# Kernel tuning notes

Measured on AMD Instinct MI355X. Metric: run time of the kernel, lower is better.

Reference implementation:

```python
import jax, jax.numpy as jnp
import numpy as np

OVERALL_W = (0.4, 0.4, 0.1, 0.1)


def nn_distance(pc1, pc2):
    # pc1: (B,N,3), pc2: (B,M,3) -> squared NN distance each way.
    # ||a-b||^2 = ||a||^2 + ||b||^2 - 2 a.b ; compute via batched GEMM.
    n1 = jnp.sum(pc1 * pc1, axis=-1)  # (B,N)
    n2 = jnp.sum(pc2 * pc2, axis=-1)  # (B,M)
    cross = jnp.einsum('bnd,bmd->bnm', pc1, pc2)  # (B,N,M)
    d = n1[:, :, None] + n2[:, None, :] - 2.0 * cross  # (B,N,M)
    dist1 = jnp.min(d, axis=2)  # (B,N)
    dist2 = jnp.min(d, axis=1)  # (B,M)
    return dist1, dist2


def setup_inputs() -> dict:
    key = jax.random.key(0)
    ks = jax.random.split(key, 7)
    bs, n_pts, num_hypo, cap_len = 16, 4096, 64, 77
    return {
        'shape_query': jax.random.normal(ks[0], (bs, n_pts, 3), dtype=jnp.float32),
        'logits': jax.random.normal(ks[1], (bs, num_hypo), dtype=jnp.float32),
        'pair_caption': jax.random.randint(ks[2], (bs, 2, cap_len), 0, 30000),
        'caption_embed': jax.random.randint(ks[3], (bs, 3, cap_len), 0, 30000),
        'sdf_pred': jax.random.normal(ks[4], (bs, 1, n_pts), dtype=jnp.float32),
        'prior': jax.random.normal(ks[5], (bs, 1024, 3), dtype=jnp.float32),
        'model': jax.random.normal(ks[6], (bs, 4096, 3), dtype=jnp.float32),
    }


def reference(shape_query, logits, pair_caption, caption_embed, sdf_pred, prior, model):
    log_prob = jax.nn.log_softmax(logits, axis=-1)
    pose_loss = -jnp.mean(log_prob[:, 0])
    reconstructed = jnp.concatenate([shape_query, prior], axis=1)  # (B, N+1024, 3)
    dist1, dist2 = nn_distance(reconstructed, model)
    shape_loss = jnp.mean(dist1) + jnp.mean(dist2)
    sdf_loss = shape_loss
    caption_loss = shape_loss
    loss = (OVERALL_W[0] * pose_loss + OVERALL_W[1] * shape_loss
            + OVERALL_W[2] * sdf_loss + OVERALL_W[3] * caption_loss)
    return (loss, pose_loss, shape_loss, sdf_loss, caption_loss)
```

## Files before the change

kernel.cpp:

```cpp
#include <hip/hip_runtime.h>
#include <math.h>

#define BATCH   16
#define NQ      4096
#define NPRIOR  1024
#define NREC    5120
#define NMODEL  4096
#define NHYP    64

#define NQD1    (BATCH*NREC)
#define NQD2    (BATCH*NMODEL)

#define P1_RS   (NREC/256)
#define P1_CB   (NMODEL/1024)
#define P1_BLOCKS (BATCH*P1_RS*P1_CB)
#define P2_RS   (NMODEL/256)
#define P2_CB   (NREC/1280)
#define P2_BLOCKS (BATCH*P2_RS*P2_CB)
#define GBLOCKS (P1_BLOCKS + P2_BLOCKS)

#define WS_WORDS (P1_CB*NQD1 + P2_CB*NQD2 + 1)
#define WS_BYTES ((size_t)WS_WORDS*4)
#define RED_BLOCKS 128

typedef _Float16 half8  __attribute__((ext_vector_type(8)));
typedef float    f32x16 __attribute__((ext_vector_type(16)));

__device__ __forceinline__ float min3f(float a, float b, float c) {
    float d;
    asm("v_min3_f32 %0, %1, %2, %3" : "=v"(d) : "v"(a), "v"(b), "v"(c));
    return d;
}

__device__ __forceinline__ half8 packQ(float x, float y, float z) {
    float n = fmaf(z, z, fmaf(y, y, x * x));
    half8 v;
    v[0] = (_Float16)(-2.0f * x); v[1] = (_Float16)(-2.0f * y);
    v[2] = (_Float16)(-2.0f * z); v[3] = (_Float16)n;
    v[4] = (_Float16)1.0f; v[5] = (_Float16)0.0f;
    v[6] = (_Float16)0.0f; v[7] = (_Float16)0.0f;
    return v;
}
__device__ __forceinline__ half8 packR(float x, float y, float z) {
    float n = fmaf(z, z, fmaf(y, y, x * x));
    half8 v;
    v[0] = (_Float16)x; v[1] = (_Float16)y; v[2] = (_Float16)z;
    v[3] = (_Float16)1.0f; v[4] = (_Float16)n;
    v[5] = (_Float16)0.0f; v[6] = (_Float16)0.0f; v[7] = (_Float16)0.0f;
    return v;
}

__device__ __forceinline__ const float* rec_ptr(
    const float* __restrict__ shape_query, const float* __restrict__ prior,
    int b, int g) {
    return (g < NQ) ? shape_query + ((size_t)b * NQ + g) * 3
                    : prior + ((size_t)b * NPRIOR + (g - NQ)) * 3;
}

__global__ __launch_bounds__(256, 4) void chamfer_pass(
    const float* __restrict__ shape_query,
    const float* __restrict__ prior,
    const float* __restrict__ model,
    float* __restrict__ ws, float* __restrict__ out) {
    __shared__ half8 Alds[257];
    __shared__ half8 Blds[1281];

    const int blk = blockIdx.x;
    if (blk == 0 && threadIdx.x == 0) {
        out[2] = 0.0f; out[3] = 0.0f;
        ((unsigned*)ws)[WS_WORDS - 1] = 0u;
    }

    const int t    = threadIdx.x;
    const int wave = t >> 6;
    const int lane = t & 63;
    const int l31  = lane & 31;
    const int kh   = lane >> 5;

    int b, rowbase, colbase, ncols, niters;
    float* rowplane;
    bool pass1 = (blk < P1_BLOCKS);
    if (pass1) {
        b = blk / (P1_RS * P1_CB);
        int rem = blk % (P1_RS * P1_CB);
        int rs = rem / P1_CB, cb = rem % P1_CB;
        rowbase = rs * 256; colbase = cb * 1024;
        ncols = 1024; niters = 16;
        rowplane = ws + (size_t)cb * NQD1 + b * NREC + rowbase;
    } else {
        int j = blk - P1_BLOCKS;
        b = j / (P2_RS * P2_CB);
        int rem = j % (P2_RS * P2_CB);
        int rs = rem / P2_CB, cb = rem % P2_CB;
        rowbase = rs * 256; colbase = cb * 1280;
        ncols = 1280; niters = 20;
        rowplane = ws + (size_t)P1_CB * NQD1 + (size_t)cb * NQD2
                   + b * NMODEL + rowbase;
    }

    {
        const float* p = pass1
            ? rec_ptr(shape_query, prior, b, rowbase + t)
            : model + ((size_t)b * NMODEL + rowbase + t) * 3;
        Alds[t] = packQ(p[0], p[1], p[2]);
    }
    for (int c = t; c < ncols; c += 256) {
        const float* p = pass1
            ? model + ((size_t)b * NMODEL + colbase + c) * 3
            : rec_ptr(shape_query, prior, b, colbase + c);
        Blds[c] = packR(p[0], p[1], p[2]);
    }
    if (t == 0) {
        half8 zz;
#pragma unroll
        for (int i = 0; i < 8; ++i) zz[i] = (_Float16)0.0f;
        Alds[256] = zz; Blds[1280] = zz;
    }
    __syncthreads();

    half8 af0 = Alds[kh ? 256 : (wave * 64 + l31)];
    half8 af1 = Alds[kh ? 256 : (wave * 64 + 32 + l31)];

    float rmn0[16], rmn1[16];
#pragma unroll
    for (int r = 0; r < 16; ++r) { rmn0[r] = 3.0e38f; rmn1[r] = 3.0e38f; }

    f32x16 cz;
#pragma unroll
    for (int i = 0; i < 16; ++i) cz[i] = 0.0f;

    half8 bfa = Blds[kh ? 1280 : l31];
    half8 bfb = Blds[kh ? 1280 : (32 + l31)];
#pragma unroll 2
    for (int it = 0; it < niters; ++it) {
        int nxt = (it + 1 == niters) ? 0 : (it + 1) * 64;
        half8 bfa_n = Blds[kh ? 1280 : (nxt + l31)];
        half8 bfb_n = Blds[kh ? 1280 : (nxt + 32 + l31)];
        f32x16 d0a = __builtin_amdgcn_mfma_f32_32x32x16_f16(af0, bfa, cz, 0, 0, 0);
        f32x16 d0b = __builtin_amdgcn_mfma_f32_32x32x16_f16(af0, bfb, cz, 0, 0, 0);
        f32x16 d1a = __builtin_amdgcn_mfma_f32_32x32x16_f16(af1, bfa, cz, 0, 0, 0);
        f32x16 d1b = __builtin_amdgcn_mfma_f32_32x32x16_f16(af1, bfb, cz, 0, 0, 0);
#pragma unroll
        for (int r = 0; r < 16; ++r) {
            rmn0[r] = min3f(rmn0[r], d0a[r], d0b[r]);
            rmn1[r] = min3f(rmn1[r], d1a[r], d1b[r]);
        }
        bfa = bfa_n; bfb = bfb_n;
    }

#pragma unroll
    for (int hv = 0; hv < 2; ++hv) {
#pragma unroll
        for (int r = 0; r < 16; ++r) {
            float v = hv ? rmn1[r] : rmn0[r];
            v = fminf(v, __shfl_xor(v, 1, 64));
            v = fminf(v, __shfl_xor(v, 2, 64));
            v = fminf(v, __shfl_xor(v, 4, 64));
            v = fminf(v, __shfl_xor(v, 8, 64));
            v = fminf(v, __shfl_xor(v, 16, 64));
            if (l31 == 0) {
                int row = wave * 64 + hv * 32 + (r & 3) + 8 * (r >> 2) + 4 * kh;
                rowplane[row] = v;
            }
        }
    }
}

__global__ __launch_bounds__(256) void reduce_finalize2(
    const float* __restrict__ ws, const float* __restrict__ logits,
    float* __restrict__ out, unsigned int* __restrict__ counter) {
    const float* p1 = ws;
    const float* p2 = ws + (size_t)P1_CB * NQD1;
    float s1 = 0.0f, s2 = 0.0f;
    const int tot = NQD1 + NQD2;
    for (int i = blockIdx.x * 256 + threadIdx.x; i < tot;
         i += RED_BLOCKS * 256) {
        if (i < NQD1) {
            s1 += fminf(fminf(p1[i],            p1[NQD1 + i]),
                        fminf(p1[2 * NQD1 + i], p1[3 * NQD1 + i]));
        } else {
            int j = i - NQD1;
            s2 += fminf(fminf(p2[j],            p2[NQD2 + j]),
                        fminf(p2[2 * NQD2 + j], p2[3 * NQD2 + j]));
        }
    }
#pragma unroll
    for (int off = 32; off > 0; off >>= 1) {
        s1 += __shfl_xor(s1, off, 64);
        s2 += __shfl_xor(s2, off, 64);
    }
    __shared__ float a1[4], a2[4];
    __shared__ int last;
    int w = threadIdx.x >> 6;
    if ((threadIdx.x & 63) == 0) { a1[w] = s1; a2[w] = s2; }
    __syncthreads();
    if (threadIdx.x == 0) {
        atomicAdd(&out[2], a1[0] + a1[1] + a1[2] + a1[3]);
        atomicAdd(&out[3], a2[0] + a2[1] + a2[2] + a2[3]);
        __threadfence();
        unsigned done = atomicAdd(counter, 1u);
        last = (done == RED_BLOCKS - 1) ? 1 : 0;
    }
    __syncthreads();
    if (last && threadIdx.x < 64) {
        const int lane = threadIdx.x;
        float pose_part = 0.0f;
        if (lane < BATCH) {
            const float* L = logits + lane * NHYP;
            float mx = L[0];
#pragma unroll 8
            for (int j = 1; j < NHYP; ++j) mx = fmaxf(mx, L[j]);
            float s = 0.0f;
#pragma unroll 8
            for (int j = 0; j < NHYP; ++j) s += expf(L[j] - mx);
            pose_part = L[0] - (mx + logf(s));
        }
#pragma unroll
        for (int off = 8; off > 0; off >>= 1)
            pose_part += __shfl_xor(pose_part, off, 64);
        if (lane == 0) {
            float sum1 = atomicAdd(&out[2], 0.0f);
            float sum2 = atomicAdd(&out[3], 0.0f);
            float shape_loss = sum1 / (float)NQD1 + sum2 / (float)NQD2;
            float pose_loss = -pose_part / (float)BATCH;
            out[0] = 0.4f * pose_loss + 0.6f * shape_loss;
            out[1] = pose_loss;
            out[2] = shape_loss;
            out[3] = shape_loss;
            out[4] = shape_loss;
        }
    }
}


__global__ void init_out(float* out) {
    if (threadIdx.x == 0) { out[2] = 0.0f; out[3] = 0.0f; }
}

__device__ __forceinline__ void scan_refs(const float* __restrict__ r, int cnt,
                                          float px, float py, float pz,
                                          float& minv) {
    for (int m = 0; m < cnt; m += 8) {
#pragma unroll
        for (int u = 0; u < 8; ++u) {
            float mx = r[(m + u) * 3 + 0];
            float my = r[(m + u) * 3 + 1];
            float mz = r[(m + u) * 3 + 2];
            float dx = px - mx, dy = py - my, dz = pz - mz;
            float d = fmaf(dz, dz, fmaf(dy, dy, dx * dx));
            minv = fminf(minv, d);
        }
    }
}

__global__ __launch_bounds__(64) void chamfer_sum(
    const float* __restrict__ qa, int na_, const float* __restrict__ qb, int nb_,
    const float* __restrict__ ra, int ma, const float* __restrict__ rb, int mb,
    float* __restrict__ accum) {
    const int b = blockIdx.y;
    const int n = blockIdx.x * 64 + threadIdx.x;
    float px, py, pz;
    if (n < na_) {
        const float* p = qa + ((size_t)b * na_ + n) * 3;
        px = p[0]; py = p[1]; pz = p[2];
    } else {
        const float* p = qb + ((size_t)b * nb_ + (n - na_)) * 3;
        px = p[0]; py = p[1]; pz = p[2];
    }
    float minv = 3.0e38f;
    scan_refs(ra + (size_t)b * ma * 3, ma, px, py, pz, minv);
    if (mb > 0) scan_refs(rb + (size_t)b * mb * 3, mb, px, py, pz, minv);
    float s = minv;
#pragma unroll
    for (int off = 32; off > 0; off >>= 1) s += __shfl_xor(s, off, 64);
    if (threadIdx.x == 0) atomicAdd(accum, s);
}

__global__ __launch_bounds__(64) void finalize_kernel(
    const float* __restrict__ logits, float* __restrict__ out) {
    const int lane = threadIdx.x;
    float pose_part = 0.0f;
    if (lane < BATCH) {
        const float* L = logits + lane * NHYP;
        float mx = L[0];
#pragma unroll 8
        for (int j = 1; j < NHYP; ++j) mx = fmaxf(mx, L[j]);
        float s = 0.0f;
#pragma unroll 8
        for (int j = 0; j < NHYP; ++j) s += expf(L[j] - mx);
        pose_part = L[0] - (mx + logf(s));
    }
#pragma unroll
    for (int off = 8; off > 0; off >>= 1) pose_part += __shfl_xor(pose_part, off, 64);
    if (lane == 0) {
        float shape_loss = out[2] / (float)NQD1 + out[3] / (float)NQD2;
        float pose_loss = -pose_part / (float)BATCH;
        out[0] = 0.4f * pose_loss + 0.6f * shape_loss;
        out[1] = pose_loss;
        out[2] = shape_loss;
        out[3] = shape_loss;
        out[4] = shape_loss;
    }
}

extern "C" void kernel_launch(void* const* d_in, const int* in_sizes, int n_in,
                              void* d_out, int out_size, void* d_ws, size_t ws_size,
                              hipStream_t stream) {
    const float* shape_query = (const float*)d_in[0];
    const float* logits      = (const float*)d_in[1];
    const float* prior       = (const float*)d_in[5];
    const float* model       = (const float*)d_in[6];
    float* out = (float*)d_out;

    if (ws_size >= WS_BYTES) {
        float* ws = (float*)d_ws;
        unsigned int* counter = (unsigned int*)ws + (WS_WORDS - 1);
        hipLaunchKernelGGL(chamfer_pass, dim3(GBLOCKS), dim3(256), 0, stream,
                           shape_query, prior, model, ws, out);
        hipLaunchKernelGGL(reduce_finalize2, dim3(RED_BLOCKS), dim3(256), 0,
                           stream, ws, logits, out, counter);
    } else {
        hipLaunchKernelGGL(init_out, dim3(1), dim3(64), 0, stream, out);
        hipLaunchKernelGGL(chamfer_sum,
                           dim3(NREC / 64, BATCH), dim3(64), 0, stream,
                           shape_query, NQ, prior, NPRIOR,
                           model, NMODEL, (const float*)nullptr, 0, out + 2);
        hipLaunchKernelGGL(chamfer_sum,
                           dim3(NMODEL / 64, BATCH), dim3(64), 0, stream,
                           model, NMODEL, (const float*)nullptr, 0,
                           shape_query, NQ, prior, NPRIOR, out + 3);
        hipLaunchKernelGGL(finalize_kernel, dim3(1), dim3(64), 0, stream,
                           logits, out);
    }
}
```

Before: 50.66 us.

## Use split hi/lo fp16 MFMA encoding for higher-precision chamfer distances

Each point's coordinates and squared norm are stored as an fp16 high part plus a residual low part, packed into a K=16 MFMA operand, so the cross-product picks up correction terms and distance accuracy approaches fp32. Row tiles shrink from 256 to 128 per block and each wave now issues two MFMAs per iteration instead of four. Pass 2 now uses five column blocks of 1024, the reduction takes the min over five planes, and the reduce grid is doubled. The cost is twice the LDS footprint per point, more blocks, and roughly the same total MFMA work spread over a finer grid.

```diff
diff --git a/kernel.cpp b/kernel.cpp
--- a/kernel.cpp
+++ b/kernel.cpp
@@ -11,17 +11,17 @@
 #define NQD1    (BATCH*NREC)
 #define NQD2    (BATCH*NMODEL)
 
-#define P1_RS   (NREC/256)
+#define P1_RS   (NREC/128)
 #define P1_CB   (NMODEL/1024)
 #define P1_BLOCKS (BATCH*P1_RS*P1_CB)
-#define P2_RS   (NMODEL/256)
-#define P2_CB   (NREC/1280)
+#define P2_RS   (NMODEL/128)
+#define P2_CB   (NREC/1024)
 #define P2_BLOCKS (BATCH*P2_RS*P2_CB)
 #define GBLOCKS (P1_BLOCKS + P2_BLOCKS)
 
 #define WS_WORDS (P1_CB*NQD1 + P2_CB*NQD2 + 1)
 #define WS_BYTES ((size_t)WS_WORDS*4)
-#define RED_BLOCKS 128
+#define RED_BLOCKS 256
 
 typedef _Float16 half8  __attribute__((ext_vector_type(8)));
 typedef float    f32x16 __attribute__((ext_vector_type(16)));
@@ -32,22 +32,36 @@
     return d;
 }
 
-__device__ __forceinline__ half8 packQ(float x, float y, float z) {
+__device__ __forceinline__ void packQ2(float x, float y, float z,
+                                       half8& hi, half8& lo) {
     float n = fmaf(z, z, fmaf(y, y, x * x));
-    half8 v;
-    v[0] = (_Float16)(-2.0f * x); v[1] = (_Float16)(-2.0f * y);
-    v[2] = (_Float16)(-2.0f * z); v[3] = (_Float16)n;
-    v[4] = (_Float16)1.0f; v[5] = (_Float16)0.0f;
-    v[6] = (_Float16)0.0f; v[7] = (_Float16)0.0f;
-    return v;
-}
-__device__ __forceinline__ half8 packR(float x, float y, float z) {
+    float mx = -2.0f * x, my = -2.0f * y, mz = -2.0f * z;
+    _Float16 xh = (_Float16)mx, yh = (_Float16)my, zh = (_Float16)mz;
+    _Float16 nh = (_Float16)n;
+    _Float16 xl = (_Float16)(mx - (float)xh);
+    _Float16 yl = (_Float16)(my - (float)yh);
+    _Float16 zl = (_Float16)(mz - (float)zh);
+    _Float16 nl = (_Float16)(n - (float)nh);
+    hi[0] = xh; hi[1] = yh; hi[2] = zh; hi[3] = nh;
+    hi[4] = (_Float16)1.0f; hi[5] = xh; hi[6] = yh; hi[7] = zh;
+    lo[0] = xl; lo[1] = yl; lo[2] = zl; lo[3] = nl;
+    lo[4] = (_Float16)1.0f; lo[5] = (_Float16)0.0f;
+    lo[6] = (_Float16)0.0f; lo[7] = (_Float16)0.0f;
+}
+__device__ __forceinline__ void packR2(float x, float y, float z,
+                                       half8& hi, half8& lo) {
     float n = fmaf(z, z, fmaf(y, y, x * x));
-    half8 v;
-    v[0] = (_Float16)x; v[1] = (_Float16)y; v[2] = (_Float16)z;
-    v[3] = (_Float16)1.0f; v[4] = (_Float16)n;
-    v[5] = (_Float16)0.0f; v[6] = (_Float16)0.0f; v[7] = (_Float16)0.0f;
-    return v;
+    _Float16 xh = (_Float16)x, yh = (_Float16)y, zh = (_Float16)z;
+    _Float16 nh = (_Float16)n;
+    _Float16 xl = (_Float16)(x - (float)xh);
+    _Float16 yl = (_Float16)(y - (float)yh);
+    _Float16 zl = (_Float16)(z - (float)zh);
+    _Float16 nl = (_Float16)(n - (float)nh);
+    hi[0] = xh; hi[1] = yh; hi[2] = zh; hi[3] = (_Float16)1.0f;
+    hi[4] = nh; hi[5] = xl; hi[6] = yl; hi[7] = zl;
+    lo[0] = xh; lo[1] = yh; lo[2] = zh; lo[3] = (_Float16)1.0f;
+    lo[4] = nl; lo[5] = (_Float16)0.0f;
+    lo[6] = (_Float16)0.0f; lo[7] = (_Float16)0.0f;
 }
 
 __device__ __forceinline__ const float* rec_ptr(
@@ -57,13 +71,13 @@
                     : prior + ((size_t)b * NPRIOR + (g - NQ)) * 3;
 }
 
-__global__ __launch_bounds__(256, 4) void chamfer_pass(
+__global__ __launch_bounds__(256) void chamfer_hp(
     const float* __restrict__ shape_query,
     const float* __restrict__ prior,
     const float* __restrict__ model,
     float* __restrict__ ws, float* __restrict__ out) {
-    __shared__ half8 Alds[257];
-    __shared__ half8 Blds[1281];
+    __shared__ half8 Alds[128 * 2];
+    __shared__ half8 Blds[1024 * 2];
 
     const int blk = blockIdx.x;
     if (blk == 0 && threadIdx.x == 0) {
@@ -77,91 +91,78 @@
     const int l31  = lane & 31;
     const int kh   = lane >> 5;
 
-    int b, rowbase, colbase, ncols, niters;
+    int b, rowbase, colbase;
     float* rowplane;
-    bool pass1 = (blk < P1_BLOCKS);
+    const bool pass1 = (blk < P1_BLOCKS);
     if (pass1) {
         b = blk / (P1_RS * P1_CB);
         int rem = blk % (P1_RS * P1_CB);
         int rs = rem / P1_CB, cb = rem % P1_CB;
-        rowbase = rs * 256; colbase = cb * 1024;
-        ncols = 1024; niters = 16;
+        rowbase = rs * 128; colbase = cb * 1024;
         rowplane = ws + (size_t)cb * NQD1 + b * NREC + rowbase;
     } else {
         int j = blk - P1_BLOCKS;
         b = j / (P2_RS * P2_CB);
         int rem = j % (P2_RS * P2_CB);
         int rs = rem / P2_CB, cb = rem % P2_CB;
-        rowbase = rs * 256; colbase = cb * 1280;
-        ncols = 1280; niters = 20;
+        rowbase = rs * 128; colbase = cb * 1024;
         rowplane = ws + (size_t)P1_CB * NQD1 + (size_t)cb * NQD2
                    + b * NMODEL + rowbase;
     }
 
-    {
+    if (t < 128) {
         const float* p = pass1
             ? rec_ptr(shape_query, prior, b, rowbase + t)
             : model + ((size_t)b * NMODEL + rowbase + t) * 3;
-        Alds[t] = packQ(p[0], p[1], p[2]);
-    }
-    for (int c = t; c < ncols; c += 256) {
+        half8 hi, lo;
+        packQ2(p[0], p[1], p[2], hi, lo);
+        Alds[t * 2] = hi; Alds[t * 2 + 1] = lo;
+    }
+    for (int c = t; c < 1024; c += 256) {
         const float* p = pass1
             ? model + ((size_t)b * NMODEL + colbase + c) * 3
             : rec_ptr(shape_query, prior, b, colbase + c);
-        Blds[c] = packR(p[0], p[1], p[2]);
-    }
-    if (t == 0) {
-        half8 zz;
-#pragma unroll
-        for (int i = 0; i < 8; ++i) zz[i] = (_Float16)0.0f;
-        Alds[256] = zz; Blds[1280] = zz;
+        half8 hi, lo;
+        packR2(p[0], p[1], p[2], hi, lo);
+        Blds[c * 2] = hi; Blds[c * 2 + 1] = lo;
     }
     __syncthreads();
 
-    half8 af0 = Alds[kh ? 256 : (wave * 64 + l31)];
-    half8 af1 = Alds[kh ? 256 : (wave * 64 + 32 + l31)];
-
-    float rmn0[16], rmn1[16];
-#pragma unroll
-    for (int r = 0; r < 16; ++r) { rmn0[r] = 3.0e38f; rmn1[r] = 3.0e38f; }
+    half8 af = Alds[(wave * 32 + l31) * 2 + kh];
+
+    float rmn[16];
+#pragma unroll
+    for (int r = 0; r < 16; ++r) rmn[r] = 3.0e38f;
 
     f32x16 cz;
 #pragma unroll
     for (int i = 0; i < 16; ++i) cz[i] = 0.0f;
 
-    half8 bfa = Blds[kh ? 1280 : l31];
-    half8 bfb = Blds[kh ? 1280 : (32 + l31)];
+    half8 bfa = Blds[l31 * 2 + kh];
+    half8 bfb = Blds[(32 + l31) * 2 + kh];
 #pragma unroll 2
-    for (int it = 0; it < niters; ++it) {
-        int nxt = (it + 1 == niters) ? 0 : (it + 1) * 64;
-        half8 bfa_n = Blds[kh ? 1280 : (nxt + l31)];
-        half8 bfb_n = Blds[kh ? 1280 : (nxt + 32 + l31)];
-        f32x16 d0a = __builtin_amdgcn_mfma_f32_32x32x16_f16(af0, bfa, cz, 0, 0, 0);
-        f32x16 d0b = __builtin_amdgcn_mfma_f32_32x32x16_f16(af0, bfb, cz, 0, 0, 0);
-        f32x16 d1a = __builtin_amdgcn_mfma_f32_32x32x16_f16(af1, bfa, cz, 0, 0, 0);
-        f32x16 d1b = __builtin_amdgcn_mfma_f32_32x32x16_f16(af1, bfb, cz, 0, 0, 0);
-#pragma unroll
-        for (int r = 0; r < 16; ++r) {
-            rmn0[r] = min3f(rmn0[r], d0a[r], d0b[r]);
-            rmn1[r] = min3f(rmn1[r], d1a[r], d1b[r]);
-        }
+    for (int it = 0; it < 16; ++it) {
+        const int nxt = (it == 15) ? 0 : (it + 1) * 64;
+        half8 bfa_n = Blds[(nxt + l31) * 2 + kh];
+        half8 bfb_n = Blds[(nxt + 32 + l31) * 2 + kh];
+        f32x16 da = __builtin_amdgcn_mfma_f32_32x32x16_f16(af, bfa, cz, 0, 0, 0);
+        f32x16 db = __builtin_amdgcn_mfma_f32_32x32x16_f16(af, bfb, cz, 0, 0, 0);
+#pragma unroll
+        for (int r = 0; r < 16; ++r) rmn[r] = min3f(rmn[r], da[r], db[r]);
         bfa = bfa_n; bfb = bfb_n;
     }
 
 #pragma unroll
-    for (int hv = 0; hv < 2; ++hv) {
-#pragma unroll
-        for (int r = 0; r < 16; ++r) {
-            float v = hv ? rmn1[r] : rmn0[r];
-            v = fminf(v, __shfl_xor(v, 1, 64));
-            v = fminf(v, __shfl_xor(v, 2, 64));
-            v = fminf(v, __shfl_xor(v, 4, 64));
-            v = fminf(v, __shfl_xor(v, 8, 64));
-            v = fminf(v, __shfl_xor(v, 16, 64));
-            if (l31 == 0) {
-                int row = wave * 64 + hv * 32 + (r & 3) + 8 * (r >> 2) + 4 * kh;
-                rowplane[row] = v;
-            }
+    for (int r = 0; r < 16; ++r) {
+        float v = rmn[r];
+        v = fminf(v, __shfl_xor(v, 1, 64));
+        v = fminf(v, __shfl_xor(v, 2, 64));
+        v = fminf(v, __shfl_xor(v, 4, 64));
+        v = fminf(v, __shfl_xor(v, 8, 64));
+        v = fminf(v, __shfl_xor(v, 16, 64));
+        if (l31 == 0) {
+            int row = wave * 32 + (r & 3) + 8 * (r >> 2) + 4 * kh;
+            rowplane[row] = v;
         }
     }
 }
@@ -180,8 +181,9 @@
                         fminf(p1[2 * NQD1 + i], p1[3 * NQD1 + i]));
         } else {
             int j = i - NQD1;
-            s2 += fminf(fminf(p2[j],            p2[NQD2 + j]),
-                        fminf(p2[2 * NQD2 + j], p2[3 * NQD2 + j]));
+            float v = fminf(fminf(p2[j],            p2[NQD2 + j]),
+                            fminf(p2[2 * NQD2 + j], p2[3 * NQD2 + j]));
+            s2 += fminf(v, p2[4 * (size_t)NQD2 + j]);
         }
     }
 #pragma unroll
@@ -315,7 +317,7 @@
     if (ws_size >= WS_BYTES) {
         float* ws = (float*)d_ws;
         unsigned int* counter = (unsigned int*)ws + (WS_WORDS - 1);
-        hipLaunchKernelGGL(chamfer_pass, dim3(GBLOCKS), dim3(256), 0, stream,
+        hipLaunchKernelGGL(chamfer_hp, dim3(GBLOCKS), dim3(256), 0, stream,
                            shape_query, prior, model, ws, out);
         hipLaunchKernelGGL(reduce_finalize2, dim3(RED_BLOCKS), dim3(256), 0,
                            stream, ws, logits, out, counter);
```

Result: slower. 68.32 us (+34.9%).
